# Kernel optimization log

Hardware: AMD Instinct MI355X
Metric: run time of the kernel (lower is better)

Reference implementation:

```python
import jax, jax.numpy as jnp
import numpy as np

B, T = 64, 512
OBS, DM, DS, NL = 115, 128, 8, 3
EMB, NA, H1 = 16, 19, 256


def _ln(x, g, b, eps=1e-5):
    m = jnp.mean(x, -1, keepdims=True)
    v = jnp.mean((x - m) ** 2, -1, keepdims=True)
    return (x - m) * jax.lax.rsqrt(v + eps) * g + b


def _s6(x, h, lng, lnb, w_ig, w_dt, b_dt, a_log, w_b, w_c, d_par, w_out):
    # x: [B,T,DM], h: [B,DM,DS]
    xn = _ln(x, lng, lnb)
    xp = xn @ w_ig.T                               # [B,T,2*DM]
    x_in, z = xp[..., :DM], xp[..., DM:]
    dt = jax.nn.softplus(x_in @ w_dt.T + b_dt)     # [B,T,DM]
    A = -jnp.exp(a_log)                            # [DM,DS]
    bt = x_in @ w_b.T                              # [B,T,DS]
    ct = x_in @ w_c.T                              # [B,T,DS]
    dA = jnp.exp(dt[..., None] * A)                # [B,T,DM,DS]
    upd = (dt * x_in)[..., None] * bt[:, :, None, :]  # [B,T,DM,DS]

    def step(hc, inp):
        dA_t, u_t, c_t = inp
        hn = dA_t * hc + u_t                       # [B,DM,DS]
        y = jnp.einsum('bds,bs->bd', hn, c_t)      # [B,DM]
        return hn, y

    h_f, ys = jax.lax.scan(
        step, h,
        (jnp.swapaxes(dA, 0, 1), jnp.swapaxes(upd, 0, 1), jnp.swapaxes(ct, 0, 1)))
    y = jnp.swapaxes(ys, 0, 1)                     # [B,T,DM]
    ssm = y * jax.nn.silu(z) + x_in * d_par
    return x + ssm @ w_out.T, h_f.reshape(h_f.shape[0], -1)


def _forward(prev_actions, obs, h0, enc_w1, enc_b1, enc_g1, enc_bb1, enc_w2, enc_b2,
             enc_g2, enc_bb2, emb, proj_w, proj_b, proj_g, proj_bb,
             m_ln_g, m_ln_b, m_w_ig, m_w_dt, m_b_dt, m_a_log, m_w_b, m_w_c, m_d, m_w_out,
             fn_g, fn_b, pol_w1, pol_b1, pol_g, pol_bb, pol_w2, pol_b2):
    # MLP encoder: Linear -> LN -> SiLU -> Linear -> LN (final norm)
    e = jax.nn.silu(_ln(obs @ enc_w1.T + enc_b1, enc_g1, enc_bb1))
    e = _ln(e @ enc_w2.T + enc_b2, enc_g2, enc_bb2)
    pa = emb[prev_actions]                         # [B,T,EMB]
    x = jnp.concatenate([e, pa], -1) @ proj_w.T + proj_b
    x = jax.nn.silu(_ln(x, proj_g, proj_bb))
    for i in range(NL):
        x, _ = _s6(x, h0[i].reshape(-1, DM, DS), m_ln_g[i], m_ln_b[i], m_w_ig[i],
                   m_w_dt[i], m_b_dt[i], m_a_log[i], m_w_b[i], m_w_c[i], m_d[i], m_w_out[i])
    x = _ln(x, fn_g, fn_b)
    p = jax.nn.silu(_ln(x @ pol_w1.T + pol_b1, pol_g, pol_bb))
    return p @ pol_w2.T + pol_b2                   # [B,T,NA] policy logits


def setup_inputs() -> dict:
    key = jax.random.key(0)
    ks = iter(jax.random.split(key, 64))
    def n(shape, s=0.05):
        return jax.random.normal(next(ks), shape, dtype=jnp.float32) * s
    return {
        'obs': jax.random.normal(next(ks), (B, T, OBS), dtype=jnp.float32),
        'h0': jnp.zeros((NL, B, DM * DS), jnp.float32),
        'enc_w1': n((H1, OBS)), 'enc_b1': jnp.zeros((H1,)),
        'enc_g1': jnp.ones((H1,)), 'enc_bb1': jnp.zeros((H1,)),
        'enc_w2': n((DM, H1)), 'enc_b2': jnp.zeros((DM,)),
        'enc_g2': jnp.ones((DM,)), 'enc_bb2': jnp.zeros((DM,)),
        'emb': n((NA + 1, EMB), 1.0),
        'proj_w': n((DM, DM + EMB)), 'proj_b': jnp.zeros((DM,)),
        'proj_g': jnp.ones((DM,)), 'proj_bb': jnp.zeros((DM,)),
        'm_ln_g': jnp.ones((NL, DM)), 'm_ln_b': jnp.zeros((NL, DM)),
        'm_w_ig': n((NL, 2 * DM, DM)), 'm_w_dt': n((NL, DM, DM)),
        'm_b_dt': jnp.zeros((NL, DM)),
        'm_a_log': jax.random.uniform(next(ks), (NL, DM, DS), minval=-3.0, maxval=-1.0, dtype=jnp.float32),
        'm_w_b': n((NL, DS, DM)), 'm_w_c': n((NL, DS, DM)),
        'm_d': jnp.ones((NL, DM)), 'm_w_out': n((NL, DM, DM)),
        'fn_g': jnp.ones((DM,)), 'fn_b': jnp.zeros((DM,)),
        'pol_w1': n((DM, DM)), 'pol_b1': jnp.zeros((DM,)),
        'pol_g': jnp.ones((DM,)), 'pol_bb': jnp.zeros((DM,)),
        'pol_w2': n((NA, DM)), 'pol_b2': jnp.zeros((NA,)),
        'prev_actions': jax.random.randint(next(ks), (B, T), 0, NA + 1),
    }


def reference(obs, h0, enc_w1, enc_b1, enc_g1, enc_bb1, enc_w2, enc_b2, enc_g2, enc_bb2,
              emb, proj_w, proj_b, proj_g, proj_bb, m_ln_g, m_ln_b, m_w_ig, m_w_dt,
              m_b_dt, m_a_log, m_w_b, m_w_c, m_d, m_w_out, fn_g, fn_b, pol_w1, pol_b1,
              pol_g, pol_bb, pol_w2, pol_b2, prev_actions):
    return _forward(prev_actions, obs, h0, enc_w1, enc_b1, enc_g1, enc_bb1, enc_w2,
                    enc_b2, enc_g2, enc_bb2, emb, proj_w, proj_b, proj_g, proj_bb,
                    m_ln_g, m_ln_b, m_w_ig, m_w_dt, m_b_dt, m_a_log, m_w_b, m_w_c,
                    m_d, m_w_out, fn_g, fn_b, pol_w1, pol_b1, pol_g, pol_bb, pol_w2, pol_b2)
```

## Files before the change

### kernel.cpp

```cpp
#include <hip/hip_runtime.h>
#include <math.h>

#define BB 64
#define TT 512
#define OBSD 115
#define DMD 128
#define DSD 8
#define NLD 3
#define EMBD 16
#define NAD 19
#define H1D 256
#define NTOK (BB*TT)
#define SSEG 16
#define TSEG (TT/SSEG)

typedef unsigned short ushort_t;
typedef __attribute__((ext_vector_type(8))) short short8;
typedef __attribute__((ext_vector_type(4))) float f32x4;

__device__ __forceinline__ float wsum(float v){
  #pragma unroll
  for (int o = 1; o < 64; o <<= 1) v += __shfl_xor(v, o, 64);
  return v;
}
__device__ __forceinline__ float silu_f(float x){ return x / (1.f + __expf(-x)); }
__device__ __forceinline__ float softplus_f(float x){
  return fmaxf(x, 0.f) + log1pf(__expf(-fabsf(x)));
}
__device__ __forceinline__ ushort_t f2bf(float x){
  unsigned u = __float_as_uint(x);
  unsigned r = (u + 0x7fffu + ((u >> 16) & 1u)) >> 16;
  return (ushort_t)r;
}
__device__ __forceinline__ float b2f(ushort_t x){
  return __uint_as_float(((unsigned)x) << 16);
}
#define MFMA(a,b,c) __builtin_amdgcn_mfma_f32_16x16x32_bf16((a),(b),(c),0,0,0)
#define LOG2E 1.44269504f

struct PJob { const float* src; ushort_t* dst; int N; int K; int Kpad; int rowofs; int Nw; };
struct PJobs { PJob j[20]; };

__global__ __launch_bounds__(256) void k_prep(PJobs P){
  const int job = blockIdx.x >> 2;
  const int sub = blockIdx.x & 3;
  PJob pj = P.j[job];
  const int elems = pj.Nw * pj.Kpad;
  for (int idx = sub*256 + threadIdx.x; idx < elems; idx += 4*256){
    int n = idx / pj.Kpad;
    int k = idx - n*pj.Kpad;
    float v = (n < pj.N && k < pj.K) ? pj.src[(size_t)n*pj.K + k] : 0.f;
    pj.dst[(size_t)(pj.rowofs + n)*pj.Kpad + k] = f2bf(v);
  }
}

__global__ __launch_bounds__(256) void k_enc1(
    const float* __restrict__ obs, const ushort_t* __restrict__ w1b,
    const float* __restrict__ b1, const float* __restrict__ g1,
    const float* __restrict__ bb1, ushort_t* __restrict__ e1)
{
  __shared__ ushort_t s_a[32*136];
  __shared__ float s_val[32*257];
  __shared__ float s_mr[32][2];
  const int tok0 = blockIdx.x * 32;
  const int tid = threadIdx.x;
  const int lane = tid & 63, w = tid >> 6;
  const int q = lane >> 4, cn = lane & 15;
  const int m0 = (w & 1) * 16, nh = w >> 1;

  for (int e = tid; e < 32*16; e += 256){
    int t = e >> 4, kc = e & 15;
    const float* op = obs + (size_t)(tok0 + t)*OBSD;
    short8 v;
    #pragma unroll
    for (int j = 0; j < 8; j++){
      int k = kc*8 + j;
      v[j] = (short)f2bf(k < OBSD ? op[k] : 0.f);
    }
    *(short8*)&s_a[t*136 + kc*8] = v;
  }
  __syncthreads();

  short8 af[4];
  #pragma unroll
  for (int ks = 0; ks < 4; ks++)
    af[ks] = *(const short8*)&s_a[(m0 + cn)*136 + ks*32 + q*8];

  #pragma unroll
  for (int nt = 0; nt < 8; nt++){
    const int n0 = (nh*8 + nt) * 16;
    f32x4 acc = {0.f,0.f,0.f,0.f};
    #pragma unroll
    for (int ks = 0; ks < 4; ks++){
      short8 bf = *(const short8*)&w1b[(size_t)(n0 + cn)*128 + ks*32 + q*8];
      acc = MFMA(af[ks], bf, acc);
    }
    float bias = b1[n0 + cn];
    #pragma unroll
    for (int r = 0; r < 4; r++)
      s_val[(m0 + q*4 + r)*257 + n0 + cn] = acc[r] + bias;
  }
  __syncthreads();

  for (int t = w*8; t < w*8 + 8; t++){
    float v0 = s_val[t*257 + lane],     v1 = s_val[t*257 + lane + 64];
    float v2 = s_val[t*257 + lane+128], v3 = s_val[t*257 + lane + 192];
    float m = wsum(v0+v1+v2+v3) * (1.f/256.f);
    float d0=v0-m, d1=v1-m, d2=v2-m, d3=v3-m;
    float var = wsum(d0*d0+d1*d1+d2*d2+d3*d3) * (1.f/256.f);
    if (lane == 0){ s_mr[t][0] = m; s_mr[t][1] = rsqrtf(var + 1e-5f); }
  }
  __syncthreads();
  for (int e = tid; e < 32*256; e += 256){
    int t = e >> 8, c = e & 255;
    float v = (s_val[t*257 + c] - s_mr[t][0]) * s_mr[t][1] * g1[c] + bb1[c];
    e1[(size_t)(tok0 + t)*256 + c] = f2bf(silu_f(v));
  }
}

__global__ __launch_bounds__(256) void k_enc2p(
    const ushort_t* __restrict__ e1, const ushort_t* __restrict__ w2b,
    const float* __restrict__ b2, const float* __restrict__ g2,
    const float* __restrict__ bb2,
    const float* __restrict__ emb, const int* __restrict__ pact,
    const ushort_t* __restrict__ pwb, const float* __restrict__ pb,
    const float* __restrict__ pg, const float* __restrict__ pbb,
    float* __restrict__ X,
    const float* __restrict__ lng, const float* __restrict__ lnb,
    const ushort_t* __restrict__ wigb, const ushort_t* __restrict__ wdbcb,
    const float* __restrict__ bdt,
    ushort_t* __restrict__ XINb, ushort_t* __restrict__ Zb,
    ushort_t* __restrict__ DTb, ushort_t* __restrict__ BTu, ushort_t* __restrict__ CTu,
    const float* __restrict__ alog0,
    float* __restrict__ HLOC, float* __restrict__ PPR)
{
  __shared__ __align__(16) char sm[45440];
  float*    s_val = (float*)sm;
  ushort_t* s_a   = (ushort_t*)(sm + 16512);
  ushort_t* s_xin = (ushort_t*)(sm + 27264);
  ushort_t* s_dt  = (ushort_t*)(sm + 35968);
  ushort_t* s_btc = (ushort_t*)(sm + 44672);
  float*    s_mr  = (float*)(sm + 45184);

  const int tok0 = blockIdx.x * 32;
  const int bidx = blockIdx.x >> 4;
  const int ch   = blockIdx.x & 15;
  const int tid = threadIdx.x;
  const int lane = tid & 63, w = tid >> 6;
  const int q = lane >> 4, cn = lane & 15;
  const int m0 = (w & 1) * 16, nh = w >> 1;

  for (int e = tid; e < 32*32; e += 256){
    int t = e >> 5, k = e & 31;
    float v = 0.f;
    if (k < EMBD){ int a = pact[tok0 + t]; v = emb[(size_t)a*EMBD + k]; }
    s_a[t*168 + 128 + k] = f2bf(v);
  }
  {
    short8 af[8];
    #pragma unroll
    for (int ks = 0; ks < 8; ks++)
      af[ks] = *(const short8*)&e1[(size_t)(tok0 + m0 + cn)*256 + ks*32 + q*8];
    #pragma unroll
    for (int nt = 0; nt < 4; nt++){
      const int n0 = (nh*4 + nt) * 16;
      f32x4 acc = {0.f,0.f,0.f,0.f};
      #pragma unroll
      for (int ks = 0; ks < 8; ks++){
        short8 bf = *(const short8*)&w2b[(size_t)(n0 + cn)*256 + ks*32 + q*8];
        acc = MFMA(af[ks], bf, acc);
      }
      float bias = b2[n0 + cn];
      #pragma unroll
      for (int r = 0; r < 4; r++)
        s_val[(m0 + q*4 + r)*129 + n0 + cn] = acc[r] + bias;
    }
  }
  __syncthreads();

  for (int t = w*8; t < w*8 + 8; t++){
    float v0 = s_val[t*129 + lane], v1 = s_val[t*129 + lane + 64];
    float m = wsum(v0+v1) * (1.f/128.f);
    float d0=v0-m, d1=v1-m;
    float var = wsum(d0*d0+d1*d1) * (1.f/128.f);
    if (lane == 0){ s_mr[t*2] = m; s_mr[t*2+1] = rsqrtf(var + 1e-5f); }
  }
  __syncthreads();
  for (int e = tid; e < 32*128; e += 256){
    int t = e >> 7, c = e & 127;
    float v = (s_val[t*129 + c] - s_mr[t*2]) * s_mr[t*2+1] * g2[c] + bb2[c];
    s_a[t*168 + c] = f2bf(v);
  }
  __syncthreads();

  {
    short8 af2[5];
    #pragma unroll
    for (int ks = 0; ks < 5; ks++)
      af2[ks] = *(const short8*)&s_a[(m0 + cn)*168 + ks*32 + q*8];
    #pragma unroll
    for (int nt = 0; nt < 4; nt++){
      const int n0 = (nh*4 + nt) * 16;
      f32x4 acc = {0.f,0.f,0.f,0.f};
      #pragma unroll
      for (int ks = 0; ks < 5; ks++){
        short8 bf = *(const short8*)&pwb[(size_t)(n0 + cn)*160 + ks*32 + q*8];
        acc = MFMA(af2[ks], bf, acc);
      }
      float bias = pb[n0 + cn];
      #pragma unroll
      for (int r = 0; r < 4; r++)
        s_val[(m0 + q*4 + r)*129 + n0 + cn] = acc[r] + bias;
    }
  }
  __syncthreads();

  for (int t = w*8; t < w*8 + 8; t++){
    float v0 = s_val[t*129 + lane], v1 = s_val[t*129 + lane + 64];
    float m = wsum(v0+v1) * (1.f/128.f);
    float d0=v0-m, d1=v1-m;
    float var = wsum(d0*d0+d1*d1) * (1.f/128.f);
    if (lane == 0){ s_mr[t*2] = m; s_mr[t*2+1] = rsqrtf(var + 1e-5f); }
  }
  __syncthreads();
  for (int e = tid; e < 32*128; e += 256){
    int t = e >> 7, c = e & 127;
    float v = (s_val[t*129 + c] - s_mr[t*2]) * s_mr[t*2+1] * pg[c] + pbb[c];
    v = silu_f(v);
    X[(size_t)tok0*128 + e] = v;
    s_val[t*129 + c] = v;
  }
  __syncthreads();

  for (int t = w*8; t < w*8 + 8; t++){
    float v0 = s_val[t*129 + lane], v1 = s_val[t*129 + lane + 64];
    float m = wsum(v0+v1) * (1.f/128.f);
    float d0=v0-m, d1=v1-m;
    float var = wsum(d0*d0+d1*d1) * (1.f/128.f);
    if (lane == 0){ s_mr[t*2] = m; s_mr[t*2+1] = rsqrtf(var + 1e-5f); }
  }
  __syncthreads();
  for (int e = tid; e < 32*128; e += 256){
    int t = e >> 7, c = e & 127;
    float v = (s_val[t*129 + c] - s_mr[t*2]) * s_mr[t*2+1] * lng[c] + lnb[c];
    s_a[t*168 + c] = f2bf(v);
  }
  __syncthreads();

  {
    short8 af[4];
    #pragma unroll
    for (int ks = 0; ks < 4; ks++)
      af[ks] = *(const short8*)&s_a[(m0 + cn)*168 + ks*32 + q*8];
    #pragma unroll
    for (int nt = 0; nt < 8; nt++){
      const int n0 = (nh*8 + nt) * 16;
      f32x4 acc = {0.f,0.f,0.f,0.f};
      #pragma unroll
      for (int ks = 0; ks < 4; ks++){
        short8 bf = *(const short8*)&wigb[(size_t)(n0 + cn)*128 + ks*32 + q*8];
        acc = MFMA(af[ks], bf, acc);
      }
      if (n0 < 128){
        #pragma unroll
        for (int r = 0; r < 4; r++){
          int tr = m0 + q*4 + r;
          ushort_t bb = f2bf(acc[r]);
          XINb[(size_t)(tok0 + tr)*128 + n0 + cn] = bb;
          s_xin[tr*136 + n0 + cn] = bb;
        }
      } else {
        #pragma unroll
        for (int r = 0; r < 4; r++){
          int tr = m0 + q*4 + r;
          Zb[(size_t)(tok0 + tr)*128 + (n0 - 128) + cn] = f2bf(acc[r]);
        }
      }
    }
  }
  __syncthreads();

  {
    short8 af2[4];
    #pragma unroll
    for (int ks = 0; ks < 4; ks++)
      af2[ks] = *(const short8*)&s_xin[(m0 + cn)*136 + ks*32 + q*8];
    for (int nt = nh; nt < 9; nt += 2){
      const int n0 = nt * 16;
      f32x4 acc = {0.f,0.f,0.f,0.f};
      #pragma unroll
      for (int ks = 0; ks < 4; ks++){
        short8 bf = *(const short8*)&wdbcb[(size_t)(n0 + cn)*128 + ks*32 + q*8];
        acc = MFMA(af2[ks], bf, acc);
      }
      const int col = n0 + cn;
      if (col < 128){
        float bd = bdt[col];
        #pragma unroll
        for (int r = 0; r < 4; r++){
          int tr = m0 + q*4 + r;
          ushort_t dv = f2bf(softplus_f(acc[r] + bd));
          DTb[(size_t)(tok0 + tr)*128 + col] = dv;
          s_dt[tr*136 + col] = dv;
        }
      } else if (col < 136){
        #pragma unroll
        for (int r = 0; r < 4; r++){
          int tr = m0 + q*4 + r;
          ushort_t bb = f2bf(acc[r]);
          BTu[(size_t)(tok0 + tr)*8 + (col - 128)] = bb;
          s_btc[tr*8 + (col - 128)] = bb;
        }
      } else {
        #pragma unroll
        for (int r = 0; r < 4; r++)
          CTu[(size_t)(tok0 + m0 + q*4 + r)*8 + (col - 136)] = f2bf(acc[r]);
      }
    }
  }
  __syncthreads();

  {
    const int d = tid & 127, sh = tid >> 7;
    float A2c[4], hh[4], pp[4];
    #pragma unroll
    for (int j = 0; j < 4; j++){
      A2c[j] = -__expf(alog0[d*8 + sh*4 + j]) * LOG2E;
      hh[j] = 0.f; pp[j] = 1.f;
    }
    for (int t = 0; t < 32; t++){
      float dt = b2f(s_dt[t*136 + d]);
      float wv = dt * b2f(s_xin[t*136 + d]);
      #pragma unroll
      for (int j = 0; j < 4; j++){
        float dA = exp2f(dt * A2c[j]);
        hh[j] = fmaf(dA, hh[j], wv * b2f(s_btc[t*8 + sh*4 + j]));
        pp[j] *= dA;
      }
    }
    const size_t o = ((size_t)bidx*16 + ch)*1024 + d*8 + sh*4;
    #pragma unroll
    for (int j = 0; j < 4; j++){ HLOC[o+j] = hh[j]; PPR[o+j] = pp[j]; }
  }
}

__global__ __launch_bounds__(256) void k_carry(
    const float* __restrict__ h0g,
    const float* __restrict__ HL, const float* __restrict__ PP,
    float* __restrict__ HST)
{
  const int b = blockIdx.x;
  const int qd = threadIdx.x;
  float4 H = *(const float4*)(h0g + (size_t)b*1024 + qd*4);
  for (int sg = 0; sg < SSEG; sg++){
    *(float4*)(HST + ((size_t)b*SSEG + sg)*1024 + qd*4) = H;
    float4 hl = *(const float4*)(HL + ((size_t)b*SSEG + sg)*1024 + qd*4);
    float4 pp = *(const float4*)(PP + ((size_t)b*SSEG + sg)*1024 + qd*4);
    H.x = fmaf(pp.x, H.x, hl.x); H.y = fmaf(pp.y, H.y, hl.y);
    H.z = fmaf(pp.z, H.z, hl.z); H.w = fmaf(pp.w, H.w, hl.w);
  }
}

__device__ __forceinline__ void phaseB_post(
    const ushort_t* DTb, const ushort_t* XINb, const ushort_t* Zb,
    const ushort_t* BTu, const ushort_t* CTu,
    const float* __restrict__ alog, const float* __restrict__ HST,
    const float* __restrict__ dpar, const ushort_t* __restrict__ woutb,
    float* __restrict__ X,
    ushort_t* s_a, float* s_x, ushort_t* s_bt, ushort_t* s_ct, float* s_mr,
    int b, int sg)
{
  const int tid = threadIdx.x;
  const int d = tid;
  const int w = tid >> 6, lane = tid & 63, q = lane >> 4, cn = lane & 15;
  const size_t segtok = (size_t)b*TT + sg*TSEG;
  const size_t rowbase = segtok*128 + d;

  ((unsigned*)s_bt)[tid] = ((const unsigned*)(BTu + segtok*8))[tid];
  ((unsigned*)s_ct)[tid] = ((const unsigned*)(CTu + segtok*8))[tid];

  float A2[8], h[8];
  #pragma unroll
  for (int s = 0; s < 8; s++){
    A2[s] = -__expf(alog[d*8 + s]) * LOG2E;
    h[s] = HST[((size_t)b*SSEG + sg)*1024 + d*8 + s];
  }
  const float dp = dpar[d];
  __syncthreads();

  const ushort_t* dtp = DTb + rowbase;
  const ushort_t* xip = XINb + rowbase;
  const ushort_t* zp  = Zb + rowbase;
  ushort_t rdt[8], rxi[8], rz[8], ndt[8], nxi[8], nz[8];
  #pragma unroll
  for (int r = 0; r < 8; r++){ rdt[r]=dtp[r*128]; rxi[r]=xip[r*128]; rz[r]=zp[r*128]; }
  for (int c = 0; c < 4; c++){
    if (c < 3){
      #pragma unroll
      for (int r = 0; r < 8; r++){
        ndt[r]=dtp[((c+1)*8+r)*128]; nxi[r]=xip[((c+1)*8+r)*128]; nz[r]=zp[((c+1)*8+r)*128];
      }
    }
    #pragma unroll
    for (int r = 0; r < 8; r++){
      const int t = c*8 + r;
      float dt = b2f(rdt[r]);
      float xi = b2f(rxi[r]);
      float wv = dt * xi;
      float y = 0.f;
      #pragma unroll
      for (int s = 0; s < 8; s++){
        float dA = exp2f(dt * A2[s]);
        h[s] = fmaf(dA, h[s], wv * b2f(s_bt[t*8 + s]));
        y = fmaf(h[s], b2f(s_ct[t*8 + s]), y);
      }
      float ssm = y * silu_f(b2f(rz[r])) + xi * dp;
      s_a[t*136 + d] = f2bf(ssm);
    }
    if (c < 3){
      #pragma unroll
      for (int r = 0; r < 8; r++){ rdt[r]=ndt[r]; rxi[r]=nxi[r]; rz[r]=nz[r]; }
    }
  }
  __syncthreads();

  {
    short8 af[2][4];
    #pragma unroll
    for (int mt = 0; mt < 2; mt++)
      #pragma unroll
      for (int ks = 0; ks < 4; ks++)
        af[mt][ks] = *(const short8*)&s_a[(mt*16 + cn)*136 + ks*32 + q*8];
    for (int nt = w; nt < 8; nt += 2){
      const int n0 = nt * 16;
      short8 bf[4];
      #pragma unroll
      for (int ks = 0; ks < 4; ks++)
        bf[ks] = *(const short8*)&woutb[(size_t)(n0+cn)*128 + ks*32 + q*8];
      #pragma unroll
      for (int mt = 0; mt < 2; mt++){
        f32x4 acc = {0.f,0.f,0.f,0.f};
        #pragma unroll
        for (int ks = 0; ks < 4; ks++) acc = MFMA(af[mt][ks], bf[ks], acc);
        #pragma unroll
        for (int r = 0; r < 4; r++){
          const int tr = mt*16 + q*4 + r;
          const size_t g = (segtok + tr)*128 + n0 + cn;
          float xn = X[g] + acc[r];
          X[g] = xn;
          s_x[tr*130 + n0 + cn] = xn;
        }
      }
    }
  }
  __syncthreads();

  {
    const int t = tid >> 2, qtr = tid & 3;
    float s = 0.f, s2 = 0.f;
    const float* row = s_x + t*130 + qtr*32;
    for (int j = 0; j < 32; j++){ float v = row[j]; s += v; s2 = fmaf(v, v, s2); }
    s  += __shfl_xor(s, 1, 64);  s2 += __shfl_xor(s2, 1, 64);
    s  += __shfl_xor(s, 2, 64);  s2 += __shfl_xor(s2, 2, 64);
    float m = s * (1.f/128.f);
    float var = s2 * (1.f/128.f) - m*m;
    if (qtr == 0){ s_mr[t*2] = m; s_mr[t*2+1] = rsqrtf(var + 1e-5f); }
  }
  __syncthreads();
}

__global__ __launch_bounds__(128) void k_scan2p(
    ushort_t* DTb, ushort_t* XINb, ushort_t* Zb,
    ushort_t* BTu, ushort_t* CTu,
    const float* __restrict__ alog, const float* __restrict__ HST,
    const float* __restrict__ dpar, const ushort_t* __restrict__ woutb,
    float* __restrict__ X,
    const float* __restrict__ lng, const float* __restrict__ lnb,
    const ushort_t* __restrict__ wigb, const ushort_t* __restrict__ wdbcb,
    const float* __restrict__ bdt,
    const float* __restrict__ alogn,
    float* __restrict__ HLOC, float* __restrict__ PPR)
{
  __shared__ __align__(16) char sm[26624];
  ushort_t* s_a  = (ushort_t*)sm;
  float*    s_x  = (float*)(sm + 8704);
  ushort_t* s_xin= (ushort_t*)(sm + 8704);
  ushort_t* s_bt = (ushort_t*)(sm + 25344);
  ushort_t* s_ct = (ushort_t*)(sm + 25856);
  float*    s_mr = (float*)(sm + 26368);

  const int b = blockIdx.x >> 4, sg = blockIdx.x & 15;
  const int tid = threadIdx.x;
  const int w = tid >> 6, lane = tid & 63, q = lane >> 4, cn = lane & 15;
  const size_t segtok = (size_t)b*TT + sg*TSEG;

  phaseB_post(DTb, XINb, Zb, BTu, CTu, alog, HST, dpar, woutb, X,
              s_a, s_x, s_bt, s_ct, s_mr, b, sg);

  {
    float g = lng[tid], c0 = lnb[tid];
    for (int t = 0; t < 32; t++){
      float v = (s_x[t*130 + tid] - s_mr[t*2]) * s_mr[t*2+1] * g + c0;
      s_a[t*136 + tid] = f2bf(v);
    }
  }
  __syncthreads();

  {
    short8 af[2][4];
    #pragma unroll
    for (int mt = 0; mt < 2; mt++)
      #pragma unroll
      for (int ks = 0; ks < 4; ks++)
        af[mt][ks] = *(const short8*)&s_a[(mt*16 + cn)*136 + ks*32 + q*8];
    for (int nt = w; nt < 16; nt += 2){
      const int n0 = nt * 16;
      short8 bf[4];
      #pragma unroll
      for (int ks = 0; ks < 4; ks++)
        bf[ks] = *(const short8*)&wigb[(size_t)(n0+cn)*128 + ks*32 + q*8];
      #pragma unroll
      for (int mt = 0; mt < 2; mt++){
        f32x4 acc = {0.f,0.f,0.f,0.f};
        #pragma unroll
        for (int ks = 0; ks < 4; ks++) acc = MFMA(af[mt][ks], bf[ks], acc);
        if (n0 < 128){
          #pragma unroll
          for (int r = 0; r < 4; r++){
            const int tr = mt*16 + q*4 + r;
            ushort_t bb = f2bf(acc[r]);
            XINb[(segtok + tr)*128 + n0 + cn] = bb;
            s_xin[tr*136 + n0 + cn] = bb;
          }
        } else {
          #pragma unroll
          for (int r = 0; r < 4; r++){
            const int tr = mt*16 + q*4 + r;
            Zb[(segtok + tr)*128 + (n0-128) + cn] = f2bf(acc[r]);
          }
        }
      }
    }
  }
  __syncthreads();

  {
    short8 af[2][4];
    #pragma unroll
    for (int mt = 0; mt < 2; mt++)
      #pragma unroll
      for (int ks = 0; ks < 4; ks++)
        af[mt][ks] = *(const short8*)&s_xin[(mt*16 + cn)*136 + ks*32 + q*8];
    for (int nt = w; nt < 9; nt += 2){
      const int n0 = nt * 16;
      short8 bf[4];
      #pragma unroll
      for (int ks = 0; ks < 4; ks++)
        bf[ks] = *(const short8*)&wdbcb[(size_t)(n0+cn)*128 + ks*32 + q*8];
      const int col = n0 + cn;
      #pragma unroll
      for (int mt = 0; mt < 2; mt++){
        f32x4 acc = {0.f,0.f,0.f,0.f};
        #pragma unroll
        for (int ks = 0; ks < 4; ks++) acc = MFMA(af[mt][ks], bf[ks], acc);
        if (col < 128){
          float bd = bdt[col];
          #pragma unroll
          for (int r = 0; r < 4; r++){
            const int tr = mt*16 + q*4 + r;
            ushort_t dv = f2bf(softplus_f(acc[r] + bd));
            DTb[(segtok + tr)*128 + col] = dv;
            s_a[tr*136 + col] = dv;
          }
        } else if (col < 136){
          #pragma unroll
          for (int r = 0; r < 4; r++){
            const int tr = mt*16 + q*4 + r;
            ushort_t bb = f2bf(acc[r]);
            BTu[(segtok + tr)*8 + (col-128)] = bb;
            s_bt[tr*8 + (col-128)] = bb;
          }
        } else {
          #pragma unroll
          for (int r = 0; r < 4; r++)
            CTu[(segtok + mt*16 + q*4 + r)*8 + (col-136)] = f2bf(acc[r]);
        }
      }
    }
  }
  __syncthreads();

  {
    float A2n[8], hh[8], pp[8];
    #pragma unroll
    for (int s = 0; s < 8; s++){
      A2n[s] = -__expf(alogn[tid*8 + s]) * LOG2E;
      hh[s] = 0.f; pp[s] = 1.f;
    }
    for (int t = 0; t < 32; t++){
      float dt = b2f(s_a[t*136 + tid]);
      float wv = dt * b2f(s_xin[t*136 + tid]);
      #pragma unroll
      for (int s = 0; s < 8; s++){
        float dA = exp2f(dt * A2n[s]);
        hh[s] = fmaf(dA, hh[s], wv * b2f(s_bt[t*8 + s]));
        pp[s] *= dA;
      }
    }
    const size_t o = ((size_t)b*SSEG + sg)*1024 + tid*8;
    #pragma unroll
    for (int s = 0; s < 8; s++){ HLOC[o+s] = hh[s]; PPR[o+s] = pp[s]; }
  }
}

__global__ __launch_bounds__(128) void k_scan2h(
    const ushort_t* DTb, const ushort_t* XINb, const ushort_t* Zb,
    const ushort_t* BTu, const ushort_t* CTu,
    const float* __restrict__ alog, const float* __restrict__ HST,
    const float* __restrict__ dpar, const ushort_t* __restrict__ woutb,
    float* __restrict__ X,
    const float* __restrict__ fng, const float* __restrict__ fnb,
    const ushort_t* __restrict__ pw1b, const float* __restrict__ pb1,
    const float* __restrict__ pg, const float* __restrict__ pbb,
    const ushort_t* __restrict__ pw2b, const float* __restrict__ pb2,
    float* __restrict__ out)
{
  __shared__ __align__(16) char sm[26624];
  ushort_t* s_a  = (ushort_t*)sm;
  float*    s_x  = (float*)(sm + 8704);
  ushort_t* s_bt = (ushort_t*)(sm + 25344);
  ushort_t* s_ct = (ushort_t*)(sm + 25856);
  float*    s_mr = (float*)(sm + 26368);

  const int b = blockIdx.x >> 4, sg = blockIdx.x & 15;
  const int tid = threadIdx.x;
  const int w = tid >> 6, lane = tid & 63, q = lane >> 4, cn = lane & 15;
  const size_t segtok = (size_t)b*TT + sg*TSEG;

  phaseB_post(DTb, XINb, Zb, BTu, CTu, alog, HST, dpar, woutb, X,
              s_a, s_x, s_bt, s_ct, s_mr, b, sg);

  {
    float g = fng[tid], c0 = fnb[tid];
    for (int t = 0; t < 32; t++){
      float v = (s_x[t*130 + tid] - s_mr[t*2]) * s_mr[t*2+1] * g + c0;
      s_a[t*136 + tid] = f2bf(v);
    }
  }
  __syncthreads();

  {
    short8 af[2][4];
    #pragma unroll
    for (int mt = 0; mt < 2; mt++)
      #pragma unroll
      for (int ks = 0; ks < 4; ks++)
        af[mt][ks] = *(const short8*)&s_a[(mt*16 + cn)*136 + ks*32 + q*8];
    for (int nt = w; nt < 8; nt += 2){
      const int n0 = nt * 16;
      short8 bf[4];
      #pragma unroll
      for (int ks = 0; ks < 4; ks++)
        bf[ks] = *(const short8*)&pw1b[(size_t)(n0+cn)*128 + ks*32 + q*8];
      float bias = pb1[n0 + cn];
      #pragma unroll
      for (int mt = 0; mt < 2; mt++){
        f32x4 acc = {0.f,0.f,0.f,0.f};
        #pragma unroll
        for (int ks = 0; ks < 4; ks++) acc = MFMA(af[mt][ks], bf[ks], acc);
        #pragma unroll
        for (int r = 0; r < 4; r++)
          s_x[(mt*16 + q*4 + r)*130 + n0 + cn] = acc[r] + bias;
      }
    }
  }
  __syncthreads();

  {
    const int t = tid >> 2, qtr = tid & 3;
    float s = 0.f, s2 = 0.f;
    const float* row = s_x + t*130 + qtr*32;
    for (int j = 0; j < 32; j++){ float v = row[j]; s += v; s2 = fmaf(v, v, s2); }
    s  += __shfl_xor(s, 1, 64);  s2 += __shfl_xor(s2, 1, 64);
    s  += __shfl_xor(s, 2, 64);  s2 += __shfl_xor(s2, 2, 64);
    float m = s * (1.f/128.f);
    float var = s2 * (1.f/128.f) - m*m;
    if (qtr == 0){ s_mr[t*2] = m; s_mr[t*2+1] = rsqrtf(var + 1e-5f); }
  }
  __syncthreads();
  {
    float g = pg[tid], c0 = pbb[tid];
    for (int t = 0; t < 32; t++){
      float v = (s_x[t*130 + tid] - s_mr[t*2]) * s_mr[t*2+1] * g + c0;
      s_a[t*136 + tid] = f2bf(silu_f(v));
    }
  }
  __syncthreads();

  {
    short8 af[2][4];
    #pragma unroll
    for (int mt = 0; mt < 2; mt++)
      #pragma unroll
      for (int ks = 0; ks < 4; ks++)
        af[mt][ks] = *(const short8*)&s_a[(mt*16 + cn)*136 + ks*32 + q*8];
    const int n0 = w * 16;
    short8 bf[4];
    #pragma unroll
    for (int ks = 0; ks < 4; ks++)
      bf[ks] = *(const short8*)&pw2b[(size_t)(n0+cn)*128 + ks*32 + q*8];
    const int col = n0 + cn;
    #pragma unroll
    for (int mt = 0; mt < 2; mt++){
      f32x4 acc = {0.f,0.f,0.f,0.f};
      #pragma unroll
      for (int ks = 0; ks < 4; ks++) acc = MFMA(af[mt][ks], bf[ks], acc);
      if (col < NAD){
        float bias = pb2[col];
        #pragma unroll
        for (int r = 0; r < 4; r++)
          out[(segtok + mt*16 + q*4 + r)*NAD + col] = acc[r] + bias;
      }
    }
  }
}

extern "C" void kernel_launch(void* const* d_in, const int* in_sizes, int n_in,
                              void* d_out, int out_size, void* d_ws, size_t ws_size,
                              hipStream_t stream) {
  const float* obs    = (const float*)d_in[0];
  const float* h0     = (const float*)d_in[1];
  const float* enc_w1 = (const float*)d_in[2];
  const float* enc_b1 = (const float*)d_in[3];
  const float* enc_g1 = (const float*)d_in[4];
  const float* enc_bb1= (const float*)d_in[5];
  const float* enc_w2 = (const float*)d_in[6];
  const float* enc_b2 = (const float*)d_in[7];
  const float* enc_g2 = (const float*)d_in[8];
  const float* enc_bb2= (const float*)d_in[9];
  const float* emb    = (const float*)d_in[10];
  const float* proj_w = (const float*)d_in[11];
  const float* proj_b = (const float*)d_in[12];
  const float* proj_g = (const float*)d_in[13];
  const float* proj_bb= (const float*)d_in[14];
  const float* m_ln_g = (const float*)d_in[15];
  const float* m_ln_b = (const float*)d_in[16];
  const float* m_w_ig = (const float*)d_in[17];
  const float* m_w_dt = (const float*)d_in[18];
  const float* m_b_dt = (const float*)d_in[19];
  const float* m_a_log= (const float*)d_in[20];
  const float* m_w_b  = (const float*)d_in[21];
  const float* m_w_c  = (const float*)d_in[22];
  const float* m_d    = (const float*)d_in[23];
  const float* m_w_out= (const float*)d_in[24];
  const float* fn_g   = (const float*)d_in[25];
  const float* fn_b   = (const float*)d_in[26];
  const float* pol_w1 = (const float*)d_in[27];
  const float* pol_b1 = (const float*)d_in[28];
  const float* pol_g  = (const float*)d_in[29];
  const float* pol_bb = (const float*)d_in[30];
  const float* pol_w2 = (const float*)d_in[31];
  const float* pol_b2 = (const float*)d_in[32];
  const int*   pact   = (const int*)d_in[33];

  float* ws  = (float*)d_ws;
  float* X    = ws;
  float* HLOC = X + (size_t)NTOK*128;
  float* PPR  = HLOC + (size_t)BB*16*1024;
  float* HST  = PPR  + (size_t)BB*16*1024;
  ushort_t* E1   = (ushort_t*)(HST + (size_t)BB*16*1024);
  ushort_t* XINb = E1   + (size_t)NTOK*256;
  ushort_t* Zb   = XINb + (size_t)NTOK*128;
  ushort_t* DTb  = Zb   + (size_t)NTOK*128;
  ushort_t* BTu  = DTb  + (size_t)NTOK*128;
  ushort_t* CTu  = BTu  + (size_t)NTOK*8;

  ushort_t* W1B   = CTu   + (size_t)NTOK*8;
  ushort_t* W2B   = W1B   + 256*128;
  ushort_t* PWB   = W2B   + 128*256;
  ushort_t* WIGB  = PWB   + 128*160;
  ushort_t* WDBCB = WIGB  + 3*256*128;
  ushort_t* WOUTB = WDBCB + 3*144*128;
  ushort_t* PW1B  = WOUTB + 3*128*128;
  ushort_t* PW2B  = PW1B  + 128*128;

  PJobs P;
  int nj = 0;
  auto add = [&](const float* src, ushort_t* dst, int N, int K, int Kpad, int rowofs, int Nw){
    P.j[nj].src = src; P.j[nj].dst = dst; P.j[nj].N = N; P.j[nj].K = K;
    P.j[nj].Kpad = Kpad; P.j[nj].rowofs = rowofs; P.j[nj].Nw = Nw; nj++;
  };
  add(enc_w1, W1B, 256, 115, 128, 0, 256);
  add(enc_w2, W2B, 128, 256, 256, 0, 128);
  add(proj_w, PWB, 128, 144, 160, 0, 128);
  for (int l = 0; l < NLD; l++)
    add(m_w_ig + (size_t)l*256*128, WIGB + (size_t)l*256*128, 256, 128, 128, 0, 256);
  for (int l = 0; l < NLD; l++){
    add(m_w_dt + (size_t)l*128*128, WDBCB + (size_t)l*144*128, 128, 128, 128, 0,   128);
    add(m_w_b  + (size_t)l*8*128,   WDBCB + (size_t)l*144*128,   8, 128, 128, 128,   8);
    add(m_w_c  + (size_t)l*8*128,   WDBCB + (size_t)l*144*128,   8, 128, 128, 136,   8);
  }
  for (int l = 0; l < NLD; l++)
    add(m_w_out + (size_t)l*128*128, WOUTB + (size_t)l*128*128, 128, 128, 128, 0, 128);
  add(pol_w1, PW1B, 128, 128, 128, 0, 128);
  add(pol_w2, PW2B,  19, 128, 128, 0,  32);

  k_prep<<<20*4, 256, 0, stream>>>(P);
  k_enc1<<<NTOK/32, 256, 0, stream>>>(obs, W1B, enc_b1, enc_g1, enc_bb1, E1);
  k_enc2p<<<NTOK/32, 256, 0, stream>>>(E1, W2B, enc_b2, enc_g2, enc_bb2,
      emb, pact, PWB, proj_b, proj_g, proj_bb, X,
      m_ln_g, m_ln_b, WIGB, WDBCB, m_b_dt,
      XINb, Zb, DTb, BTu, CTu,
      m_a_log, HLOC, PPR);

  k_carry<<<BB, 256, 0, stream>>>(h0, HLOC, PPR, HST);
  k_scan2p<<<BB*SSEG, 128, 0, stream>>>(DTb, XINb, Zb, BTu, CTu,
      m_a_log, HST, m_d, WOUTB, X,
      m_ln_g + 128, m_ln_b + 128,
      WIGB + (size_t)256*128, WDBCB + (size_t)144*128, m_b_dt + 128,
      m_a_log + 1024, HLOC, PPR);
  k_carry<<<BB, 256, 0, stream>>>(h0 + (size_t)BB*1024, HLOC, PPR, HST);
  k_scan2p<<<BB*SSEG, 128, 0, stream>>>(DTb, XINb, Zb, BTu, CTu,
      m_a_log + 1024, HST, m_d + 128, WOUTB + (size_t)128*128, X,
      m_ln_g + 256, m_ln_b + 256,
      WIGB + (size_t)2*256*128, WDBCB + (size_t)2*144*128, m_b_dt + 256,
      m_a_log + 2048, HLOC, PPR);
  k_carry<<<BB, 256, 0, stream>>>(h0 + (size_t)2*BB*1024, HLOC, PPR, HST);
  k_scan2h<<<BB*SSEG, 128, 0, stream>>>(DTb, XINb, Zb, BTu, CTu,
      m_a_log + 2048, HST, m_d + 256, WOUTB + (size_t)2*128*128, X,
      fn_g, fn_b, PW1B, pol_b1, pol_g, pol_bb, PW2B, pol_b2,
      (float*)d_out);
}
```

Baseline: 424.4 us.

## Stage scan inputs in LDS with vector loads and parallelize layernorm stats

The scan phase now loads the whole segment's dt, x_in and z tiles into shared memory with 16-byte coalesced loads, replacing per-thread strided 2-byte global loads with manual register prefetching. Layernorm statistics are computed by eight threads per token using sum and sum-of-squares with three shuffles, replacing the per-warp serial loop that did two full wave reductions per token. Shared-memory strides change to padded sizes to fit the new layout. This adds LDS footprint and switches to the single-pass variance formula, which is slightly less numerically stable.

Result: faster. 406.0 us (-4.3%).

```diff
diff --git a/kernel.cpp b/kernel.cpp
--- a/kernel.cpp
+++ b/kernel.cpp
@@ -18,11 +18,6 @@
 typedef __attribute__((ext_vector_type(8))) short short8;
 typedef __attribute__((ext_vector_type(4))) float f32x4;
 
-__device__ __forceinline__ float wsum(float v){
-  #pragma unroll
-  for (int o = 1; o < 64; o <<= 1) v += __shfl_xor(v, o, 64);
-  return v;
-}
 __device__ __forceinline__ float silu_f(float x){ return x / (1.f + __expf(-x)); }
 __device__ __forceinline__ float softplus_f(float x){
   return fmaxf(x, 0.f) + log1pf(__expf(-fabsf(x)));
@@ -37,6 +32,22 @@
 }
 #define MFMA(a,b,c) __builtin_amdgcn_mfma_f32_16x16x32_bf16((a),(b),(c),0,0,0)
 #define LOG2E 1.44269504f
+
+template<int D, int SV>
+__device__ __forceinline__ void ln32(const float* s_val, float* s_mr, int tid){
+  const int t = tid >> 3, part = tid & 7;
+  float s = 0.f, s2 = 0.f;
+  #pragma unroll
+  for (int j = part; j < D; j += 8){ float v = s_val[t*SV + j]; s += v; s2 = fmaf(v, v, s2); }
+  s += __shfl_xor(s, 1, 64); s2 += __shfl_xor(s2, 1, 64);
+  s += __shfl_xor(s, 2, 64); s2 += __shfl_xor(s2, 2, 64);
+  s += __shfl_xor(s, 4, 64); s2 += __shfl_xor(s2, 4, 64);
+  if (part == 0){
+    float m = s * (1.f/(float)D);
+    s_mr[t*2] = m;
+    s_mr[t*2+1] = rsqrtf(s2 * (1.f/(float)D) - m*m + 1e-5f);
+  }
+}
 
 struct PJob { const float* src; ushort_t* dst; int N; int K; int Kpad; int rowofs; int Nw; };
 struct PJobs { PJob j[20]; };
@@ -60,8 +71,8 @@
     const float* __restrict__ bb1, ushort_t* __restrict__ e1)
 {
   __shared__ ushort_t s_a[32*136];
-  __shared__ float s_val[32*257];
-  __shared__ float s_mr[32][2];
+  __shared__ float s_val[32*264];
+  __shared__ float s_mr[64];
   const int tok0 = blockIdx.x * 32;
   const int tid = threadIdx.x;
   const int lane = tid & 63, w = tid >> 6;
@@ -98,22 +109,15 @@
     float bias = b1[n0 + cn];
     #pragma unroll
     for (int r = 0; r < 4; r++)
-      s_val[(m0 + q*4 + r)*257 + n0 + cn] = acc[r] + bias;
-  }
-  __syncthreads();
-
-  for (int t = w*8; t < w*8 + 8; t++){
-    float v0 = s_val[t*257 + lane],     v1 = s_val[t*257 + lane + 64];
-    float v2 = s_val[t*257 + lane+128], v3 = s_val[t*257 + lane + 192];
-    float m = wsum(v0+v1+v2+v3) * (1.f/256.f);
-    float d0=v0-m, d1=v1-m, d2=v2-m, d3=v3-m;
-    float var = wsum(d0*d0+d1*d1+d2*d2+d3*d3) * (1.f/256.f);
-    if (lane == 0){ s_mr[t][0] = m; s_mr[t][1] = rsqrtf(var + 1e-5f); }
-  }
+      s_val[(m0 + q*4 + r)*264 + n0 + cn] = acc[r] + bias;
+  }
+  __syncthreads();
+
+  ln32<256,264>(s_val, s_mr, tid);
   __syncthreads();
   for (int e = tid; e < 32*256; e += 256){
     int t = e >> 8, c = e & 255;
-    float v = (s_val[t*257 + c] - s_mr[t][0]) * s_mr[t][1] * g1[c] + bb1[c];
+    float v = (s_val[t*264 + c] - s_mr[t*2]) * s_mr[t*2+1] * g1[c] + bb1[c];
     e1[(size_t)(tok0 + t)*256 + c] = f2bf(silu_f(v));
   }
 }
@@ -134,13 +138,13 @@
     const float* __restrict__ alog0,
     float* __restrict__ HLOC, float* __restrict__ PPR)
 {
-  __shared__ __align__(16) char sm[45440];
+  __shared__ __align__(16) char sm[46336];
   float*    s_val = (float*)sm;
-  ushort_t* s_a   = (ushort_t*)(sm + 16512);
-  ushort_t* s_xin = (ushort_t*)(sm + 27264);
-  ushort_t* s_dt  = (ushort_t*)(sm + 35968);
-  ushort_t* s_btc = (ushort_t*)(sm + 44672);
-  float*    s_mr  = (float*)(sm + 45184);
+  ushort_t* s_a   = (ushort_t*)(sm + 17408);
+  ushort_t* s_xin = (ushort_t*)(sm + 28160);
+  ushort_t* s_dt  = (ushort_t*)(sm + 36864);
+  ushort_t* s_btc = (ushort_t*)(sm + 45568);
+  float*    s_mr  = (float*)(sm + 46080);
 
   const int tok0 = blockIdx.x * 32;
   const int bidx = blockIdx.x >> 4;
@@ -173,22 +177,16 @@
       float bias = b2[n0 + cn];
       #pragma unroll
       for (int r = 0; r < 4; r++)
-        s_val[(m0 + q*4 + r)*129 + n0 + cn] = acc[r] + bias;
-    }
-  }
-  __syncthreads();
-
-  for (int t = w*8; t < w*8 + 8; t++){
-    float v0 = s_val[t*129 + lane], v1 = s_val[t*129 + lane + 64];
-    float m = wsum(v0+v1) * (1.f/128.f);
-    float d0=v0-m, d1=v1-m;
-    float var = wsum(d0*d0+d1*d1) * (1.f/128.f);
-    if (lane == 0){ s_mr[t*2] = m; s_mr[t*2+1] = rsqrtf(var + 1e-5f); }
-  }
+        s_val[(m0 + q*4 + r)*136 + n0 + cn] = acc[r] + bias;
+    }
+  }
+  __syncthreads();
+
+  ln32<128,136>(s_val, s_mr, tid);
   __syncthreads();
   for (int e = tid; e < 32*128; e += 256){
     int t = e >> 7, c = e & 127;
-    float v = (s_val[t*129 + c] - s_mr[t*2]) * s_mr[t*2+1] * g2[c] + bb2[c];
+    float v = (s_val[t*136 + c] - s_mr[t*2]) * s_mr[t*2+1] * g2[c] + bb2[c];
     s_a[t*168 + c] = f2bf(v);
   }
   __syncthreads();
@@ -210,39 +208,27 @@
       float bias = pb[n0 + cn];
       #pragma unroll
       for (int r = 0; r < 4; r++)
-        s_val[(m0 + q*4 + r)*129 + n0 + cn] = acc[r] + bias;
-    }
-  }
-  __syncthreads();
-
-  for (int t = w*8; t < w*8 + 8; t++){
-    float v0 = s_val[t*129 + lane], v1 = s_val[t*129 + lane + 64];
-    float m = wsum(v0+v1) * (1.f/128.f);
-    float d0=v0-m, d1=v1-m;
-    float var = wsum(d0*d0+d1*d1) * (1.f/128.f);
-    if (lane == 0){ s_mr[t*2] = m; s_mr[t*2+1] = rsqrtf(var + 1e-5f); }
-  }
+        s_val[(m0 + q*4 + r)*136 + n0 + cn] = acc[r] + bias;
+    }
+  }
+  __syncthreads();
+
+  ln32<128,136>(s_val, s_mr, tid);
   __syncthreads();
   for (int e = tid; e < 32*128; e += 256){
     int t = e >> 7, c = e & 127;
-    float v = (s_val[t*129 + c] - s_mr[t*2]) * s_mr[t*2+1] * pg[c] + pbb[c];
+    float v = (s_val[t*136 + c] - s_mr[t*2]) * s_mr[t*2+1] * pg[c] + pbb[c];
     v = silu_f(v);
     X[(size_t)tok0*128 + e] = v;
-    s_val[t*129 + c] = v;
-  }
-  __syncthreads();
-
-  for (int t = w*8; t < w*8 + 8; t++){
-    float v0 = s_val[t*129 + lane], v1 = s_val[t*129 + lane + 64];
-    float m = wsum(v0+v1) * (1.f/128.f);
-    float d0=v0-m, d1=v1-m;
-    float var = wsum(d0*d0+d1*d1) * (1.f/128.f);
-    if (lane == 0){ s_mr[t*2] = m; s_mr[t*2+1] = rsqrtf(var + 1e-5f); }
-  }
+    s_val[t*136 + c] = v;
+  }
+  __syncthreads();
+
+  ln32<128,136>(s_val, s_mr, tid);
   __syncthreads();
   for (int e = tid; e < 32*128; e += 256){
     int t = e >> 7, c = e & 127;
-    float v = (s_val[t*129 + c] - s_mr[t*2]) * s_mr[t*2+1] * lng[c] + lnb[c];
+    float v = (s_val[t*136 + c] - s_mr[t*2]) * s_mr[t*2+1] * lng[c] + lnb[c];
     s_a[t*168 + c] = f2bf(v);
   }
   __syncthreads();
@@ -361,24 +347,42 @@
   }
 }
 
+#define SMS 34560
+
 __device__ __forceinline__ void phaseB_post(
     const ushort_t* DTb, const ushort_t* XINb, const ushort_t* Zb,
     const ushort_t* BTu, const ushort_t* CTu,
     const float* __restrict__ alog, const float* __restrict__ HST,
     const float* __restrict__ dpar, const ushort_t* __restrict__ woutb,
-    float* __restrict__ X,
-    ushort_t* s_a, float* s_x, ushort_t* s_bt, ushort_t* s_ct, float* s_mr,
-    int b, int sg)
+    float* __restrict__ X, char* sm, int b, int sg)
 {
+  ushort_t* s_dtS = (ushort_t*)sm;
+  ushort_t* s_xiS = (ushort_t*)(sm + 8192);
+  ushort_t* s_zS  = (ushort_t*)(sm + 16384);
+  ushort_t* s_a   = (ushort_t*)(sm + 24576);
+  float*    s_x   = (float*)sm;
+  ushort_t* s_bt  = (ushort_t*)(sm + 33280);
+  ushort_t* s_ct  = (ushort_t*)(sm + 33792);
+  float*    s_mr  = (float*)(sm + 34304);
+
   const int tid = threadIdx.x;
   const int d = tid;
   const int w = tid >> 6, lane = tid & 63, q = lane >> 4, cn = lane & 15;
   const size_t segtok = (size_t)b*TT + sg*TSEG;
-  const size_t rowbase = segtok*128 + d;
-
-  ((unsigned*)s_bt)[tid] = ((const unsigned*)(BTu + segtok*8))[tid];
-  ((unsigned*)s_ct)[tid] = ((const unsigned*)(CTu + segtok*8))[tid];
-
+
+  {
+    const uint4* gdt = (const uint4*)(DTb + segtok*128);
+    const uint4* gxi = (const uint4*)(XINb + segtok*128);
+    const uint4* gz  = (const uint4*)(Zb + segtok*128);
+    #pragma unroll
+    for (int i = 0; i < 4; i++){
+      ((uint4*)s_dtS)[tid + i*128] = gdt[tid + i*128];
+      ((uint4*)s_xiS)[tid + i*128] = gxi[tid + i*128];
+      ((uint4*)s_zS )[tid + i*128] = gz [tid + i*128];
+    }
+    ((unsigned*)s_bt)[tid] = ((const unsigned*)(BTu + segtok*8))[tid];
+    ((unsigned*)s_ct)[tid] = ((const unsigned*)(CTu + segtok*8))[tid];
+  }
   float A2[8], h[8];
   #pragma unroll
   for (int s = 0; s < 8; s++){
@@ -388,39 +392,20 @@
   const float dp = dpar[d];
   __syncthreads();
 
-  const ushort_t* dtp = DTb + rowbase;
-  const ushort_t* xip = XINb + rowbase;
-  const ushort_t* zp  = Zb + rowbase;
-  ushort_t rdt[8], rxi[8], rz[8], ndt[8], nxi[8], nz[8];
-  #pragma unroll
-  for (int r = 0; r < 8; r++){ rdt[r]=dtp[r*128]; rxi[r]=xip[r*128]; rz[r]=zp[r*128]; }
-  for (int c = 0; c < 4; c++){
-    if (c < 3){
-      #pragma unroll
-      for (int r = 0; r < 8; r++){
-        ndt[r]=dtp[((c+1)*8+r)*128]; nxi[r]=xip[((c+1)*8+r)*128]; nz[r]=zp[((c+1)*8+r)*128];
-      }
-    }
-    #pragma unroll
-    for (int r = 0; r < 8; r++){
-      const int t = c*8 + r;
-      float dt = b2f(rdt[r]);
-      float xi = b2f(rxi[r]);
-      float wv = dt * xi;
-      float y = 0.f;
-      #pragma unroll
-      for (int s = 0; s < 8; s++){
-        float dA = exp2f(dt * A2[s]);
-        h[s] = fmaf(dA, h[s], wv * b2f(s_bt[t*8 + s]));
-        y = fmaf(h[s], b2f(s_ct[t*8 + s]), y);
-      }
-      float ssm = y * silu_f(b2f(rz[r])) + xi * dp;
-      s_a[t*136 + d] = f2bf(ssm);
-    }
-    if (c < 3){
-      #pragma unroll
-      for (int r = 0; r < 8; r++){ rdt[r]=ndt[r]; rxi[r]=nxi[r]; rz[r]=nz[r]; }
-    }
+  #pragma unroll 4
+  for (int t = 0; t < 32; t++){
+    float dt = b2f(s_dtS[t*128 + d]);
+    float xi = b2f(s_xiS[t*128 + d]);
+    float wv = dt * xi;
+    float y = 0.f;
+    #pragma unroll
+    for (int s = 0; s < 8; s++){
+      float dA = exp2f(dt * A2[s]);
+      h[s] = fmaf(dA, h[s], wv * b2f(s_bt[t*8 + s]));
+      y = fmaf(h[s], b2f(s_ct[t*8 + s]), y);
+    }
+    float ssm = y * silu_f(b2f(s_zS[t*128 + d])) + xi * dp;
+    s_a[t*136 + d] = f2bf(ssm);
   }
   __syncthreads();
 
@@ -481,21 +466,19 @@
     const float* __restrict__ alogn,
     float* __restrict__ HLOC, float* __restrict__ PPR)
 {
-  __shared__ __align__(16) char sm[26624];
-  ushort_t* s_a  = (ushort_t*)sm;
-  float*    s_x  = (float*)(sm + 8704);
-  ushort_t* s_xin= (ushort_t*)(sm + 8704);
-  ushort_t* s_bt = (ushort_t*)(sm + 25344);
-  ushort_t* s_ct = (ushort_t*)(sm + 25856);
-  float*    s_mr = (float*)(sm + 26368);
+  __shared__ __align__(16) char sm[SMS];
+  ushort_t* s_a  = (ushort_t*)(sm + 24576);
+  float*    s_x  = (float*)sm;
+  ushort_t* s_xin= (ushort_t*)sm;
+  ushort_t* s_bt = (ushort_t*)(sm + 33280);
+  float*    s_mr = (float*)(sm + 34304);
 
   const int b = blockIdx.x >> 4, sg = blockIdx.x & 15;
   const int tid = threadIdx.x;
   const int w = tid >> 6, lane = tid & 63, q = lane >> 4, cn = lane & 15;
   const size_t segtok = (size_t)b*TT + sg*TSEG;
 
-  phaseB_post(DTb, XINb, Zb, BTu, CTu, alog, HST, dpar, woutb, X,
-              s_a, s_x, s_bt, s_ct, s_mr, b, sg);
+  phaseB_post(DTb, XINb, Zb, BTu, CTu, alog, HST, dpar, woutb, X, sm, b, sg);
 
   {
     float g = lng[tid], c0 = lnb[tid];
@@ -625,20 +608,18 @@
     const ushort_t* __restrict__ pw2b, const float* __restrict__ pb2,
     float* __restrict__ out)
 {
-  __shared__ __align__(16) char sm[26624];
-  ushort_t* s_a  = (ushort_t*)sm;
-  float*    s_x  = (float*)(sm + 8704);
-  ushort_t* s_bt = (ushort_t*)(sm + 25344);
-  ushort_t* s_ct = (ushort_t*)(sm + 25856);
-  float*    s_mr = (float*)(sm + 26368);
+  __shared__ __align__(16) char sm[SMS];
+  ushort_t* s_a  = (ushort_t*)(sm + 24576);
+  float*    s_x  = (float*)sm;
+  float*    s_mr = (float*)(sm + 34304);
 
   const int b = blockIdx.x >> 4, sg = blockIdx.x & 15;
   const int tid = threadIdx.x;
   const int w = tid >> 6, lane = tid & 63, q = lane >> 4, cn = lane & 15;
   const size_t segtok = (size_t)b*TT + sg*TSEG;
 
-  phaseB_post(DTb, XINb, Zb, BTu, CTu, alog, HST, dpar, woutb, X,
-              s_a, s_x, s_bt, s_ct, s_mr, b, sg);
+  phaseB_post((ushort_t*)DTb, (ushort_t*)XINb, (ushort_t*)Zb,
+              (ushort_t*)BTu, (ushort_t*)CTu, alog, HST, dpar, woutb, X, sm, b, sg);
 
   {
     float g = fng[tid], c0 = fnb[tid];
```
